# Kernel tuning notes

Measured on AMD Instinct MI355X. Metric: run time of the kernel, lower is better.

Reference implementation:

```python
import jax, jax.numpy as jnp
import numpy as np

N_NODES = 50000
N_EDGES = 640000
HID = 128


def _lin_params(key, out_dim, in_dim):
    kw, kb = jax.random.split(key)
    W = jax.random.normal(kw, (out_dim, in_dim), dtype=jnp.float32) * 0.02
    b = jax.random.normal(kb, (out_dim,), dtype=jnp.float32) * 0.02
    return W, b


def setup_inputs() -> dict:
    key = jax.random.key(0)
    ks = jax.random.split(key, 12)
    x = jax.random.normal(ks[0], (N_NODES, 3), dtype=jnp.float32)
    h = jax.random.normal(ks[1], (N_NODES, HID), dtype=jnp.float32)
    edge_index = jax.random.randint(ks[2], (2, N_EDGES), 0, N_NODES, dtype=jnp.int64)
    # edge_mlp: Linear(2H+1,H) -> SiLU -> Linear(H,H) -> SiLU -> Linear(H,H)
    ew1, eb1 = _lin_params(ks[3], HID, 2 * HID + 1)
    ew2, eb2 = _lin_params(ks[4], HID, HID)
    ew3, eb3 = _lin_params(ks[5], HID, HID)
    # coord_mlp: Linear(H,H) -> SiLU -> Linear(H,1)
    cw1, cb1 = _lin_params(ks[6], HID, HID)
    cw2, cb2 = _lin_params(ks[7], 1, HID)
    # node_mlp: Linear(2H,H) -> SiLU -> Linear(H,H) -> SiLU -> Linear(H,H)
    nw1, nb1 = _lin_params(ks[8], HID, 2 * HID)
    nw2, nb2 = _lin_params(ks[9], HID, HID)
    nw3, nb3 = _lin_params(ks[10], HID, HID)
    return {
        "x": x, "h": h, "edge_index": edge_index,
        "ew1": ew1, "eb1": eb1, "ew2": ew2, "eb2": eb2, "ew3": ew3, "eb3": eb3,
        "cw1": cw1, "cb1": cb1, "cw2": cw2, "cb2": cb2,
        "nw1": nw1, "nb1": nb1, "nw2": nw2, "nb2": nb2, "nw3": nw3, "nb3": nb3,
    }


def _lin(z, W, b):
    return z @ W.T + b


def _mlp3(z, W1, b1, W2, b2, W3, b3):
    z = jax.nn.silu(_lin(z, W1, b1))
    z = jax.nn.silu(_lin(z, W2, b2))
    return _lin(z, W3, b3)


def reference(x, h, edge_index,
              ew1, eb1, ew2, eb2, ew3, eb3,
              cw1, cb1, cw2, cb2,
              nw1, nb1, nw2, nb2, nw3, nb3):
    n = h.shape[0]
    src, dst = edge_index[0], edge_index[1]
    rel = x[src] - x[dst]                                   # [E, 3]
    d2 = jnp.sum(rel * rel, axis=-1, keepdims=True)         # [E, 1]
    e_in = jnp.concatenate([h[src], h[dst], d2], axis=-1)   # [E, 2H+1]
    m_ij = _mlp3(e_in, ew1, eb1, ew2, eb2, ew3, eb3)        # [E, H]
    m_aggr = jax.ops.segment_sum(m_ij, src, num_segments=n)  # [N, H]
    coord_coef = jnp.tanh(_lin(jax.nn.silu(_lin(m_ij, cw1, cb1)), cw2, cb2))  # [E, 1]
    delta_x = jax.ops.segment_sum(rel * coord_coef, src, num_segments=n)      # [N, 3]
    x_out = x + delta_x
    h_out = h + _mlp3(jnp.concatenate([h, m_aggr], axis=-1), nw1, nb1, nw2, nb2, nw3, nb3)
    return (x_out, h_out)
```

## Files before the change

### kernel.cpp

```cpp
#include <hip/hip_runtime.h>
#include <hip/hip_bf16.h>

#define N_NODES 50000
#define N_EDGES 640000
#define HID 128

typedef unsigned short ushort_t;
typedef __attribute__((ext_vector_type(8))) short bf16x8;
typedef __attribute__((ext_vector_type(4))) float f32x4;

#define U_MAGGR 0
#define U_HB    6400000
#define U_W1B   12800000
#define U_W2B   12832768
#define U_W3B   12849152
#define U_C1B   12865536
#define U_N1B   12881920
#define U_N2B   12914688
#define U_N3B   12931072
#define U_W1D2  12947456

__device__ __forceinline__ float silu_f(float v) {
    const float e = __builtin_amdgcn_exp2f(v * -1.442695041f);
    return v * __builtin_amdgcn_rcpf(1.0f + e);
}

__device__ __forceinline__ ushort_t f2b(float f) {
    __hip_bfloat16 b = __float2bfloat16(f);
    return __builtin_bit_cast(ushort_t, b);
}
__device__ __forceinline__ float b2f(ushort_t u) {
    union { float f; unsigned int i; } v; v.i = ((unsigned int)u) << 16; return v.f;
}
__device__ __forceinline__ float u2f(unsigned int u) {
    union { float f; unsigned int i; } v; v.i = u; return v.f;
}
__device__ __forceinline__ unsigned int pack2(float a, float b) {
    return (unsigned int)f2b(a) | ((unsigned int)f2b(b) << 16);
}
__device__ __forceinline__ void up8(const uint4& u, float* f) {
    f[0] = u2f(u.x << 16); f[1] = u2f(u.x & 0xffff0000u);
    f[2] = u2f(u.y << 16); f[3] = u2f(u.y & 0xffff0000u);
    f[4] = u2f(u.z << 16); f[5] = u2f(u.z & 0xffff0000u);
    f[6] = u2f(u.w << 16); f[7] = u2f(u.w & 0xffff0000u);
}
__device__ __forceinline__ void atom_add_f32(float* p, float v) { unsafeAtomicAdd(p, v); }

__device__ __forceinline__ void atom_pk_bf16(ushort_t* p, unsigned int v) {
#if __has_builtin(__builtin_amdgcn_global_atomic_fadd_v2bf16)
    typedef __attribute__((ext_vector_type(2))) short s2;
    s2 sv = __builtin_bit_cast(s2, v);
    __builtin_amdgcn_global_atomic_fadd_v2bf16((__attribute__((address_space(1))) s2*)p, sv);
#else
    unsigned int* up = (unsigned int*)p;
    unsigned int old = __hip_atomic_load(up, __ATOMIC_RELAXED, __HIP_MEMORY_SCOPE_AGENT), assumed;
    do {
        assumed = old;
        float lo = b2f((ushort_t)(assumed & 0xffff)) + b2f((ushort_t)(v & 0xffff));
        float hi = b2f((ushort_t)(assumed >> 16)) + b2f((ushort_t)(v >> 16));
        unsigned int nv = (unsigned int)f2b(lo) | ((unsigned int)f2b(hi) << 16);
        old = atomicCAS(up, assumed, nv);
    } while (old != assumed);
#endif
}

__global__ void prep_kernel(const float* __restrict__ x, const float* __restrict__ h,
                            const float* __restrict__ ew1, const float* __restrict__ ew2,
                            const float* __restrict__ ew3, const float* __restrict__ cw1,
                            const float* __restrict__ nw1, const float* __restrict__ nw2,
                            const float* __restrict__ nw3,
                            ushort_t* __restrict__ wsu, float* __restrict__ xout) {
    long i = (long)blockIdx.x * 256 + threadIdx.x;
    if (i < 3200000) { ((unsigned int*)(wsu + U_MAGGR))[i] = 0u; return; }
    i -= 3200000;
    if (i < 3200000) { ((unsigned int*)(wsu + U_HB))[i] = pack2(h[2 * i], h[2 * i + 1]); return; }
    i -= 3200000;
    if (i < 32768) {
        const int f = (int)(i >> 7);
        const int k = (int)(i & 127);
        const int src = (f < 128) ? (f * 257 + k) : ((f - 128) * 257 + 128 + k);
        wsu[U_W1B + i] = f2b(ew1[src]);
        return;
    }
    i -= 32768;
    if (i < 16384) { wsu[U_W2B + i] = f2b(ew2[i]); return; }
    i -= 16384;
    if (i < 16384) { wsu[U_W3B + i] = f2b(ew3[i]); return; }
    i -= 16384;
    if (i < 16384) { wsu[U_C1B + i] = f2b(cw1[i]); return; }
    i -= 16384;
    if (i < 32768) { wsu[U_N1B + i] = f2b(nw1[i]); return; }
    i -= 32768;
    if (i < 16384) { wsu[U_N2B + i] = f2b(nw2[i]); return; }
    i -= 16384;
    if (i < 16384) { wsu[U_N3B + i] = f2b(nw3[i]); return; }
    i -= 16384;
    if (i < 128) { ((float*)(wsu + U_W1D2))[i] = ew1[i * 257 + 256]; return; }
    i -= 128;
    if (i < 150000) xout[i] = x[i];
}

__global__ __launch_bounds__(256, 4) void ab_kernel(
    const ushort_t* __restrict__ hb, const ushort_t* __restrict__ wab,
    const float* __restrict__ eb1, ushort_t* __restrict__ abp) {
    __shared__ ushort_t sH[8192];
    const int t = threadIdx.x;
    const int lane = t & 63;
    const int wid = t >> 6;
    const int r15 = lane & 15;
    const int khi = lane >> 4;
    const int rhi = khi * 4;
    const int fb = wid * 64;
    const int n0 = blockIdx.x * 64;

    const uint4* hb4 = (const uint4*)hb;
#pragma unroll
    for (int it = 0; it < 4; ++it) {
        const int idx = it * 256 + t;
        const int e = idx >> 4, c = idx & 15;
        const int n = n0 + e;
        uint4 v = make_uint4(0u, 0u, 0u, 0u);
        if (n < N_NODES) v = hb4[(size_t)n * 16 + c];
        const int ui = (e * 128 + c * 8) ^ ((e & 7) << 3);
        *(uint4*)(sH + ui) = v;
    }
    __syncthreads();

    f32x4 acc[4][4];
#pragma unroll
    for (int mi = 0; mi < 4; ++mi)
#pragma unroll
        for (int ni = 0; ni < 4; ++ni) acc[mi][ni] = (f32x4){0.f, 0.f, 0.f, 0.f};
#pragma unroll
    for (int ks = 0; ks < 4; ++ks) {
        bf16x8 a[4];
#pragma unroll
        for (int mi = 0; mi < 4; ++mi)
            a[mi] = *(const bf16x8*)(wab + (fb + mi * 16 + r15) * 128 + ks * 32 + khi * 8);
        bf16x8 b[4];
#pragma unroll
        for (int ni = 0; ni < 4; ++ni) {
            const int e = ni * 16 + r15;
            const int ui = (e * 128 + ks * 32 + khi * 8) ^ ((e & 7) << 3);
            b[ni] = *(const bf16x8*)(sH + ui);
        }
#pragma unroll
        for (int mi = 0; mi < 4; ++mi)
#pragma unroll
            for (int ni = 0; ni < 4; ++ni)
                acc[mi][ni] = __builtin_amdgcn_mfma_f32_16x16x32_bf16(a[mi], b[ni], acc[mi][ni], 0, 0, 0);
    }

#pragma unroll
    for (int mi = 0; mi < 4; ++mi) {
        const int f0 = fb + mi * 16 + rhi;
        float4 bb = make_float4(0.f, 0.f, 0.f, 0.f);
        if (f0 >= 128) bb = *(const float4*)&eb1[f0 - 128];
#pragma unroll
        for (int ni = 0; ni < 4; ++ni) {
            const int n = n0 + ni * 16 + r15;
            if (n < N_NODES) {
                *(uint2*)(abp + (size_t)n * 256 + f0) =
                    make_uint2(pack2(acc[mi][ni][0] + bb.x, acc[mi][ni][1] + bb.y),
                               pack2(acc[mi][ni][2] + bb.z, acc[mi][ni][3] + bb.w));
            }
        }
    }
}

template <bool ACT>
__device__ __forceinline__ void dense128(ushort_t* sE, int srcBase, int dstBase,
                                         const ushort_t* __restrict__ W,
                                         const float* __restrict__ bias,
                                         int r15, int khi, int rhi, int fb) {
    f32x4 acc[4];
#pragma unroll
    for (int ni = 0; ni < 4; ++ni) acc[ni] = (f32x4){0.f, 0.f, 0.f, 0.f};
#pragma unroll
    for (int ks = 0; ks < 4; ++ks) {
        const bf16x8 a0 = *(const bf16x8*)(W + (fb + r15) * 128 + ks * 32 + khi * 8);
        bf16x8 b[4];
#pragma unroll
        for (int ni = 0; ni < 4; ++ni) {
            const int edge = ni * 16 + r15;
            const int ui = (srcBase + edge * 128 + ks * 32 + khi * 8) ^ ((edge & 7) << 3);
            b[ni] = *(const bf16x8*)(sE + ui);
        }
#pragma unroll
        for (int ni = 0; ni < 4; ++ni)
            acc[ni] = __builtin_amdgcn_mfma_f32_16x16x32_bf16(a0, b[ni], acc[ni], 0, 0, 0);
    }
    const float4 bb = *(const float4*)&bias[fb + rhi];
#pragma unroll
    for (int ni = 0; ni < 4; ++ni) {
        const int edge = ni * 16 + r15;
        float v0 = acc[ni][0] + bb.x;
        float v1 = acc[ni][1] + bb.y;
        float v2 = acc[ni][2] + bb.z;
        float v3 = acc[ni][3] + bb.w;
        if (ACT) { v0 = silu_f(v0); v1 = silu_f(v1); v2 = silu_f(v2); v3 = silu_f(v3); }
        const int ui = (dstBase + edge * 128 + fb + rhi) ^ ((edge & 7) << 3);
        *(uint2*)(sE + ui) = make_uint2(pack2(v0, v1), pack2(v2, v3));
    }
}

__global__ __launch_bounds__(512, 8) void edge_kernel(
    const float* __restrict__ x, const ushort_t* __restrict__ ab,
    const int* __restrict__ ei,
    const float* __restrict__ w1d2,
    const ushort_t* __restrict__ w2b, const float* __restrict__ eb2,
    const ushort_t* __restrict__ w3b, const float* __restrict__ eb3,
    const ushort_t* __restrict__ c1b, const float* __restrict__ cb1,
    const float* __restrict__ cw2, const float* __restrict__ cb2,
    float* __restrict__ xout, ushort_t* __restrict__ maggr) {
    __shared__ ushort_t sE[16384];
    __shared__ float srel[64][3];
    __shared__ float sd2[64];
    __shared__ int ssrc[64];
    __shared__ int sdst[64];

    const int t = threadIdx.x;
    const int lane = t & 63;
    const int wid = t >> 6;
    const int r15 = lane & 15;
    const int khi = lane >> 4;
    const int rhi = khi * 4;
    const int fb = wid * 16;
    const int e0 = blockIdx.x * 64;

    if (t < 64) {
        const int s = ei[e0 + t], d = ei[N_EDGES + e0 + t];
        ssrc[t] = s; sdst[t] = d;
        const float rx = x[3 * s] - x[3 * d];
        const float ry = x[3 * s + 1] - x[3 * d + 1];
        const float rz = x[3 * s + 2] - x[3 * d + 2];
        srel[t][0] = rx; srel[t][1] = ry; srel[t][2] = rz;
        sd2[t] = rx * rx + ry * ry + rz * rz;
    }
    __syncthreads();

    {
        const uint4* ab4 = (const uint4*)ab;
        uint4 va[2], vb[2];
        int ui[2], cc[2];
        float dd[2];
#pragma unroll
        for (int it = 0; it < 2; ++it) {
            const int idx = it * 512 + t;
            const int e = idx >> 4, c = idx & 15;
            va[it] = ab4[(size_t)ssrc[e] * 32 + c];
            vb[it] = ab4[(size_t)sdst[e] * 32 + 16 + c];
            dd[it] = sd2[e];
            cc[it] = c;
            ui[it] = (e * 128 + c * 8) ^ ((e & 7) << 3);
        }
#pragma unroll
        for (int it = 0; it < 2; ++it) {
            const int c8 = cc[it] * 8;
            const float4 w0 = *(const float4*)&w1d2[c8];
            const float4 w1 = *(const float4*)&w1d2[c8 + 4];
            const float d2 = dd[it];
            float fa[8], fbv[8];
            up8(va[it], fa);
            up8(vb[it], fbv);
            const float v0 = silu_f(fmaf(d2, w0.x, fa[0] + fbv[0]));
            const float v1 = silu_f(fmaf(d2, w0.y, fa[1] + fbv[1]));
            const float v2 = silu_f(fmaf(d2, w0.z, fa[2] + fbv[2]));
            const float v3 = silu_f(fmaf(d2, w0.w, fa[3] + fbv[3]));
            const float v4 = silu_f(fmaf(d2, w1.x, fa[4] + fbv[4]));
            const float v5 = silu_f(fmaf(d2, w1.y, fa[5] + fbv[5]));
            const float v6 = silu_f(fmaf(d2, w1.z, fa[6] + fbv[6]));
            const float v7 = silu_f(fmaf(d2, w1.w, fa[7] + fbv[7]));
            uint4 st;
            st.x = pack2(v0, v1); st.y = pack2(v2, v3);
            st.z = pack2(v4, v5); st.w = pack2(v6, v7);
            *(uint4*)(sE + ui[it]) = st;
        }
    }
    __syncthreads();

    dense128<true >(sE, 0, 8192, w2b, eb2, r15, khi, rhi, fb);
    __syncthreads();
    dense128<false>(sE, 8192, 0, w3b, eb3, r15, khi, rhi, fb);
    __syncthreads();
    dense128<true >(sE, 0, 8192, c1b, cb1, r15, khi, rhi, fb);
    __syncthreads();

    {
        const int esub = lane & 7;
        const int kg = lane >> 3;
        const int edge = wid * 8 + esub;
        float sum = 0.f;
#pragma unroll
        for (int cc = 0; cc < 2; ++cc) {
            const int k = kg * 16 + cc * 8;
            const int ui = (8192 + edge * 128 + k) ^ (esub << 3);
            const bf16x8 v = *(const bf16x8*)(sE + ui);
            const float4 ca = *(const float4*)&cw2[k];
            const float4 cb = *(const float4*)&cw2[k + 4];
            sum = fmaf(b2f((ushort_t)v[0]), ca.x, sum);
            sum = fmaf(b2f((ushort_t)v[1]), ca.y, sum);
            sum = fmaf(b2f((ushort_t)v[2]), ca.z, sum);
            sum = fmaf(b2f((ushort_t)v[3]), ca.w, sum);
            sum = fmaf(b2f((ushort_t)v[4]), cb.x, sum);
            sum = fmaf(b2f((ushort_t)v[5]), cb.y, sum);
            sum = fmaf(b2f((ushort_t)v[6]), cb.z, sum);
            sum = fmaf(b2f((ushort_t)v[7]), cb.w, sum);
        }
        sum += __shfl_xor(sum, 8);
        sum += __shfl_xor(sum, 16);
        sum += __shfl_xor(sum, 32);
        if (kg == 0) {
            const float coef = tanhf(sum + cb2[0]);
            const int s = ssrc[edge];
            atom_add_f32(&xout[3 * s + 0], srel[edge][0] * coef);
            atom_add_f32(&xout[3 * s + 1], srel[edge][1] * coef);
            atom_add_f32(&xout[3 * s + 2], srel[edge][2] * coef);
        }
    }

    {
        unsigned int v[8];
        size_t gaddr[8];
#pragma unroll
        for (int it = 0; it < 8; ++it) {
            const int idx = it * 512 + t;
            const int e = idx >> 6;
            const int dw = idx & 63;
            const int ui = (e * 128 + dw * 2) ^ ((e & 7) << 3);
            v[it] = *(const unsigned int*)(sE + ui);
            gaddr[it] = (size_t)ssrc[e] * 128 + dw * 2;
        }
#pragma unroll
        for (int it = 0; it < 8; ++it) atom_pk_bf16(maggr + gaddr[it], v[it]);
    }
}

__global__ __launch_bounds__(256, 4) void node_kernel(
    const float* __restrict__ h, const ushort_t* __restrict__ hb,
    const ushort_t* __restrict__ maggr,
    const ushort_t* __restrict__ n1b, const float* __restrict__ nb1,
    const ushort_t* __restrict__ n2b, const float* __restrict__ nb2,
    const ushort_t* __restrict__ n3b, const float* __restrict__ nb3,
    float* __restrict__ hout) {
    __shared__ ushort_t sE[16384];
    const int t = threadIdx.x;
    const int lane = t & 63;
    const int wid = t >> 6;
    const int r15 = lane & 15;
    const int khi = lane >> 4;
    const int rhi = khi * 4;
    const int fb = wid * 32;
    const int n0 = blockIdx.x * 64;

    const uint4* hb4 = (const uint4*)hb;
    const uint4* mg4 = (const uint4*)maggr;
#pragma unroll
    for (int it = 0; it < 8; ++it) {
        const int idx = it * 256 + t;
        const int e = idx >> 5, c = idx & 31;
        const int n = n0 + e;
        uint4 v = make_uint4(0u, 0u, 0u, 0u);
        if (n < N_NODES) v = (c < 16) ? hb4[(size_t)n * 16 + c] : mg4[(size_t)n * 16 + (c - 16)];
        const int ui = (e * 256 + c * 8) ^ ((e & 7) << 3);
        *(uint4*)(sE + ui) = v;
    }
    __syncthreads();

    f32x4 acc[2][4];
#pragma unroll
    for (int mi = 0; mi < 2; ++mi)
#pragma unroll
        for (int ni = 0; ni < 4; ++ni) acc[mi][ni] = (f32x4){0.f, 0.f, 0.f, 0.f};
#pragma unroll
    for (int ks = 0; ks < 8; ++ks) {
        const bf16x8 a0 = *(const bf16x8*)(n1b + (fb + r15) * 256 + ks * 32 + khi * 8);
        const bf16x8 a1 = *(const bf16x8*)(n1b + (fb + 16 + r15) * 256 + ks * 32 + khi * 8);
        bf16x8 b[4];
#pragma unroll
        for (int ni = 0; ni < 4; ++ni) {
            const int edge = ni * 16 + r15;
            const int ui = (edge * 256 + ks * 32 + khi * 8) ^ ((edge & 7) << 3);
            b[ni] = *(const bf16x8*)(sE + ui);
        }
#pragma unroll
        for (int ni = 0; ni < 4; ++ni) {
            acc[0][ni] = __builtin_amdgcn_mfma_f32_16x16x32_bf16(a0, b[ni], acc[0][ni], 0, 0, 0);
            acc[1][ni] = __builtin_amdgcn_mfma_f32_16x16x32_bf16(a1, b[ni], acc[1][ni], 0, 0, 0);
        }
    }
    __syncthreads();
    {
        const float4 bb0 = *(const float4*)&nb1[fb + rhi];
        const float4 bb1 = *(const float4*)&nb1[fb + 16 + rhi];
#pragma unroll
        for (int mi = 0; mi < 2; ++mi) {
            const float4 bb = mi ? bb1 : bb0;
#pragma unroll
            for (int ni = 0; ni < 4; ++ni) {
                const int edge = ni * 16 + r15;
                const float v0 = silu_f(acc[mi][ni][0] + bb.x);
                const float v1 = silu_f(acc[mi][ni][1] + bb.y);
                const float v2 = silu_f(acc[mi][ni][2] + bb.z);
                const float v3 = silu_f(acc[mi][ni][3] + bb.w);
                const int ui = (edge * 128 + fb + mi * 16 + rhi) ^ ((edge & 7) << 3);
                *(uint2*)(sE + ui) = make_uint2(pack2(v0, v1), pack2(v2, v3));
            }
        }
    }
    __syncthreads();

    {
#pragma unroll
        for (int half = 0; half < 2; ++half) {
            f32x4 a2[4];
#pragma unroll
            for (int ni = 0; ni < 4; ++ni) a2[ni] = (f32x4){0.f, 0.f, 0.f, 0.f};
            const int fbh = fb + half * 16;
#pragma unroll
            for (int ks = 0; ks < 4; ++ks) {
                const bf16x8 a0 = *(const bf16x8*)(n2b + (fbh + r15) * 128 + ks * 32 + khi * 8);
                bf16x8 b[4];
#pragma unroll
                for (int ni = 0; ni < 4; ++ni) {
                    const int edge = ni * 16 + r15;
                    const int ui = (edge * 128 + ks * 32 + khi * 8) ^ ((edge & 7) << 3);
                    b[ni] = *(const bf16x8*)(sE + ui);
                }
#pragma unroll
                for (int ni = 0; ni < 4; ++ni)
                    a2[ni] = __builtin_amdgcn_mfma_f32_16x16x32_bf16(a0, b[ni], a2[ni], 0, 0, 0);
            }
            const float4 bb = *(const float4*)&nb2[fbh + rhi];
#pragma unroll
            for (int ni = 0; ni < 4; ++ni) {
                const int edge = ni * 16 + r15;
                const float v0 = silu_f(a2[ni][0] + bb.x);
                const float v1 = silu_f(a2[ni][1] + bb.y);
                const float v2 = silu_f(a2[ni][2] + bb.z);
                const float v3 = silu_f(a2[ni][3] + bb.w);
                const int ui = (8192 + edge * 128 + fbh + rhi) ^ ((edge & 7) << 3);
                *(uint2*)(sE + ui) = make_uint2(pack2(v0, v1), pack2(v2, v3));
            }
        }
    }
    __syncthreads();

    {
        f32x4 a3[2][4];
#pragma unroll
        for (int mi = 0; mi < 2; ++mi)
#pragma unroll
            for (int ni = 0; ni < 4; ++ni) a3[mi][ni] = (f32x4){0.f, 0.f, 0.f, 0.f};
#pragma unroll
        for (int ks = 0; ks < 4; ++ks) {
            const bf16x8 a0 = *(const bf16x8*)(n3b + (fb + r15) * 128 + ks * 32 + khi * 8);
            const bf16x8 a1 = *(const bf16x8*)(n3b + (fb + 16 + r15) * 128 + ks * 32 + khi * 8);
            bf16x8 b[4];
#pragma unroll
            for (int ni = 0; ni < 4; ++ni) {
                const int edge = ni * 16 + r15;
                const int ui = (8192 + edge * 128 + ks * 32 + khi * 8) ^ ((edge & 7) << 3);
                b[ni] = *(const bf16x8*)(sE + ui);
            }
#pragma unroll
            for (int ni = 0; ni < 4; ++ni) {
                a3[0][ni] = __builtin_amdgcn_mfma_f32_16x16x32_bf16(a0, b[ni], a3[0][ni], 0, 0, 0);
                a3[1][ni] = __builtin_amdgcn_mfma_f32_16x16x32_bf16(a1, b[ni], a3[1][ni], 0, 0, 0);
            }
        }
        const float4 bb0 = *(const float4*)&nb3[fb + rhi];
        const float4 bb1 = *(const float4*)&nb3[fb + 16 + rhi];
#pragma unroll
        for (int mi = 0; mi < 2; ++mi) {
            const float4 bb = mi ? bb1 : bb0;
#pragma unroll
            for (int ni = 0; ni < 4; ++ni) {
                const int n = n0 + ni * 16 + r15;
                if (n < N_NODES) {
                    const size_t o = (size_t)n * 128 + fb + mi * 16 + rhi;
                    const float4 hv = *(const float4*)&h[o];
                    float4 ov;
                    ov.x = hv.x + a3[mi][ni][0] + bb.x;
                    ov.y = hv.y + a3[mi][ni][1] + bb.y;
                    ov.z = hv.z + a3[mi][ni][2] + bb.z;
                    ov.w = hv.w + a3[mi][ni][3] + bb.w;
                    *(float4*)&hout[o] = ov;
                }
            }
        }
    }
}

extern "C" void kernel_launch(void* const* d_in, const int* in_sizes, int n_in,
                              void* d_out, int out_size, void* d_ws, size_t ws_size,
                              hipStream_t stream) {
    const float* x   = (const float*)d_in[0];
    const float* h   = (const float*)d_in[1];
    const int*   ei  = (const int*)d_in[2];
    const float* ew1 = (const float*)d_in[3];
    const float* eb1 = (const float*)d_in[4];
    const float* ew2 = (const float*)d_in[5];
    const float* eb2 = (const float*)d_in[6];
    const float* ew3 = (const float*)d_in[7];
    const float* eb3 = (const float*)d_in[8];
    const float* cw1 = (const float*)d_in[9];
    const float* cb1 = (const float*)d_in[10];
    const float* cw2 = (const float*)d_in[11];
    const float* cb2 = (const float*)d_in[12];
    const float* nw1 = (const float*)d_in[13];
    const float* nb1 = (const float*)d_in[14];
    const float* nw2 = (const float*)d_in[15];
    const float* nb2 = (const float*)d_in[16];
    const float* nw3 = (const float*)d_in[17];
    const float* nb3 = (const float*)d_in[18];

    float* out  = (float*)d_out;
    float* xout = out;
    float* hout = out + (size_t)N_NODES * 3;
    ushort_t* wsu = (ushort_t*)d_ws;

    ushort_t* maggr = wsu + U_MAGGR;
    const ushort_t* hb  = wsu + U_HB;
    const ushort_t* wab = wsu + U_W1B;
    const ushort_t* w2b = wsu + U_W2B;
    const ushort_t* w3b = wsu + U_W3B;
    const ushort_t* c1b = wsu + U_C1B;
    const ushort_t* n1b = wsu + U_N1B;
    const ushort_t* n2b = wsu + U_N2B;
    const ushort_t* n3b = wsu + U_N3B;
    const float* w1d2 = (const float*)(wsu + U_W1D2);

    ushort_t* abp = (ushort_t*)hout;

    const long prep_total = 3200000L + 3200000L + 32768 + 3 * 16384 + 32768 + 2 * 16384 + 128 + 150000;
    const int prep_blocks = (int)((prep_total + 255) / 256);
    prep_kernel<<<prep_blocks, 256, 0, stream>>>(x, h, ew1, ew2, ew3, cw1, nw1, nw2, nw3,
                                                 wsu, xout);

    ab_kernel<<<(N_NODES + 63) / 64, 256, 0, stream>>>(hb, wab, eb1, abp);

    edge_kernel<<<N_EDGES / 64, 512, 0, stream>>>(x, abp, ei,
                                                  w1d2, w2b, eb2, w3b, eb3,
                                                  c1b, cb1, cw2, cb2,
                                                  xout, maggr);

    node_kernel<<<(N_NODES + 63) / 64, 256, 0, stream>>>(h, hb, maggr,
                                                         n1b, nb1, n2b, nb2, n3b, nb3,
                                                         hout);
}
```

Before: 315.6 us.

## Fold edge layer-3 weights into coord MLP and scatter messages straight from MFMA accumulators

Since m_ij = W3·z + b3 feeds the coord MLP linearly, the change precomputes Wc = C1·W3 and bc = C1·b3 + cb1 in an extra block of ab_kernel. That lets the edge kernel compute the W3 layer and the coord layer from the same layer-2 activations without a dependent round trip through shared memory. The layer-3 output is atomically added to maggr directly from the MFMA accumulators, and the coord dot product is reduced in registers with a small shared partial buffer instead of a separate LDS pass. Edge index and gather loads are also issued before the first barrier to overlap latency. The cost is an extra block with a 128x128 matmul, a larger LDS footprint in ab_kernel, and slightly different bf16 rounding for the coord path.

```diff
diff --git a/kernel.cpp b/kernel.cpp
--- a/kernel.cpp
+++ b/kernel.cpp
@@ -19,6 +19,8 @@
 #define U_N2B   12914688
 #define U_N3B   12931072
 #define U_W1D2  12947456
+#define U_WC    12947712
+#define U_BC    12964096
 
 __device__ __forceinline__ float silu_f(float v) {
     const float e = __builtin_amdgcn_exp2f(v * -1.442695041f);
@@ -102,14 +104,68 @@
 
 __global__ __launch_bounds__(256, 4) void ab_kernel(
     const ushort_t* __restrict__ hb, const ushort_t* __restrict__ wab,
-    const float* __restrict__ eb1, ushort_t* __restrict__ abp) {
-    __shared__ ushort_t sH[8192];
+    const float* __restrict__ eb1, ushort_t* __restrict__ abp,
+    const ushort_t* __restrict__ c1b, const float* __restrict__ ew3,
+    const float* __restrict__ eb3, const float* __restrict__ cb1,
+    ushort_t* __restrict__ wcb, float* __restrict__ bcv, int nAB) {
+    __shared__ ushort_t sH[16384];
     const int t = threadIdx.x;
     const int lane = t & 63;
     const int wid = t >> 6;
     const int r15 = lane & 15;
     const int khi = lane >> 4;
     const int rhi = khi * 4;
+
+    if ((int)blockIdx.x == nAB) {
+        for (int i = t; i < 16384; i += 256) {
+            const int m = i >> 7, k = i & 127;
+            sH[(k * 128 + m) ^ ((k & 7) << 3)] = f2b(ew3[i]);
+        }
+        __syncthreads();
+#pragma unroll
+        for (int kh = 0; kh < 2; ++kh) {
+#pragma unroll
+            for (int fi = 0; fi < 2; ++fi) {
+                const int f0 = wid * 32 + fi * 16;
+                const int kc = kh * 64;
+                f32x4 acc[4];
+#pragma unroll
+                for (int ni = 0; ni < 4; ++ni) acc[ni] = (f32x4){0.f, 0.f, 0.f, 0.f};
+#pragma unroll
+                for (int ks = 0; ks < 4; ++ks) {
+                    const bf16x8 a0 = *(const bf16x8*)(c1b + (f0 + r15) * 128 + ks * 32 + khi * 8);
+                    bf16x8 b[4];
+#pragma unroll
+                    for (int ni = 0; ni < 4; ++ni) {
+                        const int kk = kc + ni * 16 + r15;
+                        b[ni] = *(const bf16x8*)(sH + ((kk * 128 + ks * 32 + khi * 8) ^ ((kk & 7) << 3)));
+                    }
+#pragma unroll
+                    for (int ni = 0; ni < 4; ++ni)
+                        acc[ni] = __builtin_amdgcn_mfma_f32_16x16x32_bf16(a0, b[ni], acc[ni], 0, 0, 0);
+                }
+#pragma unroll
+                for (int ni = 0; ni < 4; ++ni) {
+                    const int kk = kc + ni * 16 + r15;
+#pragma unroll
+                    for (int j = 0; j < 4; ++j)
+                        wcb[(f0 + rhi + j) * 128 + kk] = f2b(acc[ni][j]);
+                }
+            }
+        }
+        {
+            const int f = t >> 1, hf = t & 1;
+            float s = 0.f;
+            const int m0 = hf * 64;
+#pragma unroll 8
+            for (int m = m0; m < m0 + 64; ++m)
+                s = fmaf(b2f(c1b[f * 128 + m]), eb3[m], s);
+            s += __shfl_xor(s, 1);
+            if (hf == 0) bcv[f] = cb1[f] + s;
+        }
+        return;
+    }
+
     const int fb = wid * 64;
     const int n0 = blockIdx.x * 64;
 
@@ -210,14 +266,14 @@
     const float* __restrict__ w1d2,
     const ushort_t* __restrict__ w2b, const float* __restrict__ eb2,
     const ushort_t* __restrict__ w3b, const float* __restrict__ eb3,
-    const ushort_t* __restrict__ c1b, const float* __restrict__ cb1,
+    const ushort_t* __restrict__ wcb, const float* __restrict__ bcv,
     const float* __restrict__ cw2, const float* __restrict__ cb2,
     float* __restrict__ xout, ushort_t* __restrict__ maggr) {
     __shared__ ushort_t sE[16384];
     __shared__ float srel[64][3];
     __shared__ float sd2[64];
     __shared__ int ssrc[64];
-    __shared__ int sdst[64];
+    __shared__ float sPart[8][64];
 
     const int t = threadIdx.x;
     const int lane = t & 63;
@@ -228,9 +284,25 @@
     const int fb = wid * 16;
     const int e0 = blockIdx.x * 64;
 
+    uint4 va[2], vb[2];
+    int ui[2], ee[2];
+    {
+        const uint4* ab4 = (const uint4*)ab;
+#pragma unroll
+        for (int it = 0; it < 2; ++it) {
+            const int idx = it * 512 + t;
+            const int e = idx >> 4, c = idx & 15;
+            const int s = ei[e0 + e];
+            const int d = ei[N_EDGES + e0 + e];
+            va[it] = ab4[(size_t)s * 32 + c];
+            vb[it] = ab4[(size_t)d * 32 + 16 + c];
+            ee[it] = e;
+            ui[it] = (e * 128 + c * 8) ^ ((e & 7) << 3);
+        }
+    }
     if (t < 64) {
         const int s = ei[e0 + t], d = ei[N_EDGES + e0 + t];
-        ssrc[t] = s; sdst[t] = d;
+        ssrc[t] = s;
         const float rx = x[3 * s] - x[3 * d];
         const float ry = x[3 * s + 1] - x[3 * d + 1];
         const float rz = x[3 * s + 2] - x[3 * d + 2];
@@ -239,100 +311,113 @@
     }
     __syncthreads();
 
+#pragma unroll
+    for (int it = 0; it < 2; ++it) {
+        const int c8 = ((it * 512 + t) & 15) * 8;
+        const float4 w0 = *(const float4*)&w1d2[c8];
+        const float4 w1 = *(const float4*)&w1d2[c8 + 4];
+        const float d2 = sd2[ee[it]];
+        float fa[8], fbv[8];
+        up8(va[it], fa);
+        up8(vb[it], fbv);
+        const float v0 = silu_f(fmaf(d2, w0.x, fa[0] + fbv[0]));
+        const float v1 = silu_f(fmaf(d2, w0.y, fa[1] + fbv[1]));
+        const float v2 = silu_f(fmaf(d2, w0.z, fa[2] + fbv[2]));
+        const float v3 = silu_f(fmaf(d2, w0.w, fa[3] + fbv[3]));
+        const float v4 = silu_f(fmaf(d2, w1.x, fa[4] + fbv[4]));
+        const float v5 = silu_f(fmaf(d2, w1.y, fa[5] + fbv[5]));
+        const float v6 = silu_f(fmaf(d2, w1.z, fa[6] + fbv[6]));
+        const float v7 = silu_f(fmaf(d2, w1.w, fa[7] + fbv[7]));
+        uint4 st;
+        st.x = pack2(v0, v1); st.y = pack2(v2, v3);
+        st.z = pack2(v4, v5); st.w = pack2(v6, v7);
+        *(uint4*)(sE + ui[it]) = st;
+    }
+    __syncthreads();
+
+    dense128<true>(sE, 0, 8192, w2b, eb2, r15, khi, rhi, fb);
+    __syncthreads();
+
     {
-        const uint4* ab4 = (const uint4*)ab;
-        uint4 va[2], vb[2];
-        int ui[2], cc[2];
-        float dd[2];
-#pragma unroll
-        for (int it = 0; it < 2; ++it) {
-            const int idx = it * 512 + t;
-            const int e = idx >> 4, c = idx & 15;
-            va[it] = ab4[(size_t)ssrc[e] * 32 + c];
-            vb[it] = ab4[(size_t)sdst[e] * 32 + 16 + c];
-            dd[it] = sd2[e];
-            cc[it] = c;
-            ui[it] = (e * 128 + c * 8) ^ ((e & 7) << 3);
-        }
-#pragma unroll
-        for (int it = 0; it < 2; ++it) {
-            const int c8 = cc[it] * 8;
-            const float4 w0 = *(const float4*)&w1d2[c8];
-            const float4 w1 = *(const float4*)&w1d2[c8 + 4];
-            const float d2 = dd[it];
-            float fa[8], fbv[8];
-            up8(va[it], fa);
-            up8(vb[it], fbv);
-            const float v0 = silu_f(fmaf(d2, w0.x, fa[0] + fbv[0]));
-            const float v1 = silu_f(fmaf(d2, w0.y, fa[1] + fbv[1]));
-            const float v2 = silu_f(fmaf(d2, w0.z, fa[2] + fbv[2]));
-            const float v3 = silu_f(fmaf(d2, w0.w, fa[3] + fbv[3]));
-            const float v4 = silu_f(fmaf(d2, w1.x, fa[4] + fbv[4]));
-            const float v5 = silu_f(fmaf(d2, w1.y, fa[5] + fbv[5]));
-            const float v6 = silu_f(fmaf(d2, w1.z, fa[6] + fbv[6]));
-            const float v7 = silu_f(fmaf(d2, w1.w, fa[7] + fbv[7]));
-            uint4 st;
-            st.x = pack2(v0, v1); st.y = pack2(v2, v3);
-            st.z = pack2(v4, v5); st.w = pack2(v6, v7);
-            *(uint4*)(sE + ui[it]) = st;
-        }
-    }
-    __syncthreads();
-
-    dense128<true >(sE, 0, 8192, w2b, eb2, r15, khi, rhi, fb);
-    __syncthreads();
-    dense128<false>(sE, 8192, 0, w3b, eb3, r15, khi, rhi, fb);
-    __syncthreads();
-    dense128<true >(sE, 0, 8192, c1b, cb1, r15, khi, rhi, fb);
-    __syncthreads();
+        f32x4 acc[4];
+#pragma unroll
+        for (int ni = 0; ni < 4; ++ni) acc[ni] = (f32x4){0.f, 0.f, 0.f, 0.f};
+#pragma unroll
+        for (int ks = 0; ks < 4; ++ks) {
+            const bf16x8 a0 = *(const bf16x8*)(w3b + (fb + r15) * 128 + ks * 32 + khi * 8);
+            bf16x8 b[4];
+#pragma unroll
+            for (int ni = 0; ni < 4; ++ni) {
+                const int edge = ni * 16 + r15;
+                const int u = (8192 + edge * 128 + ks * 32 + khi * 8) ^ ((edge & 7) << 3);
+                b[ni] = *(const bf16x8*)(sE + u);
+            }
+#pragma unroll
+            for (int ni = 0; ni < 4; ++ni)
+                acc[ni] = __builtin_amdgcn_mfma_f32_16x16x32_bf16(a0, b[ni], acc[ni], 0, 0, 0);
+        }
+        const float4 bb = *(const float4*)&eb3[fb + rhi];
+#pragma unroll
+        for (int ni = 0; ni < 4; ++ni) {
+            const int edge = ni * 16 + r15;
+            const unsigned int w0 = pack2(acc[ni][0] + bb.x, acc[ni][1] + bb.y);
+            const unsigned int w1 = pack2(acc[ni][2] + bb.z, acc[ni][3] + bb.w);
+            const size_t g = (size_t)ssrc[edge] * 128 + fb + rhi;
+            atom_pk_bf16(maggr + g, w0);
+            atom_pk_bf16(maggr + g + 2, w1);
+        }
+    }
 
     {
-        const int esub = lane & 7;
-        const int kg = lane >> 3;
-        const int edge = wid * 8 + esub;
-        float sum = 0.f;
-#pragma unroll
-        for (int cc = 0; cc < 2; ++cc) {
-            const int k = kg * 16 + cc * 8;
-            const int ui = (8192 + edge * 128 + k) ^ (esub << 3);
-            const bf16x8 v = *(const bf16x8*)(sE + ui);
-            const float4 ca = *(const float4*)&cw2[k];
-            const float4 cb = *(const float4*)&cw2[k + 4];
-            sum = fmaf(b2f((ushort_t)v[0]), ca.x, sum);
-            sum = fmaf(b2f((ushort_t)v[1]), ca.y, sum);
-            sum = fmaf(b2f((ushort_t)v[2]), ca.z, sum);
-            sum = fmaf(b2f((ushort_t)v[3]), ca.w, sum);
-            sum = fmaf(b2f((ushort_t)v[4]), cb.x, sum);
-            sum = fmaf(b2f((ushort_t)v[5]), cb.y, sum);
-            sum = fmaf(b2f((ushort_t)v[6]), cb.z, sum);
-            sum = fmaf(b2f((ushort_t)v[7]), cb.w, sum);
-        }
-        sum += __shfl_xor(sum, 8);
-        sum += __shfl_xor(sum, 16);
-        sum += __shfl_xor(sum, 32);
-        if (kg == 0) {
-            const float coef = tanhf(sum + cb2[0]);
-            const int s = ssrc[edge];
-            atom_add_f32(&xout[3 * s + 0], srel[edge][0] * coef);
-            atom_add_f32(&xout[3 * s + 1], srel[edge][1] * coef);
-            atom_add_f32(&xout[3 * s + 2], srel[edge][2] * coef);
-        }
-    }
-
-    {
-        unsigned int v[8];
-        size_t gaddr[8];
-#pragma unroll
-        for (int it = 0; it < 8; ++it) {
-            const int idx = it * 512 + t;
-            const int e = idx >> 6;
-            const int dw = idx & 63;
-            const int ui = (e * 128 + dw * 2) ^ ((e & 7) << 3);
-            v[it] = *(const unsigned int*)(sE + ui);
-            gaddr[it] = (size_t)ssrc[e] * 128 + dw * 2;
-        }
-#pragma unroll
-        for (int it = 0; it < 8; ++it) atom_pk_bf16(maggr + gaddr[it], v[it]);
+        f32x4 acc[4];
+#pragma unroll
+        for (int ni = 0; ni < 4; ++ni) acc[ni] = (f32x4){0.f, 0.f, 0.f, 0.f};
+#pragma unroll
+        for (int ks = 0; ks < 4; ++ks) {
+            const bf16x8 a0 = *(const bf16x8*)(wcb + (fb + r15) * 128 + ks * 32 + khi * 8);
+            bf16x8 b[4];
+#pragma unroll
+            for (int ni = 0; ni < 4; ++ni) {
+                const int edge = ni * 16 + r15;
+                const int u = (8192 + edge * 128 + ks * 32 + khi * 8) ^ ((edge & 7) << 3);
+                b[ni] = *(const bf16x8*)(sE + u);
+            }
+#pragma unroll
+            for (int ni = 0; ni < 4; ++ni)
+                acc[ni] = __builtin_amdgcn_mfma_f32_16x16x32_bf16(a0, b[ni], acc[ni], 0, 0, 0);
+        }
+        const float4 bb = *(const float4*)&bcv[fb + rhi];
+        const float4 cw = *(const float4*)&cw2[fb + rhi];
+        float p[4];
+#pragma unroll
+        for (int ni = 0; ni < 4; ++ni) {
+            float s = silu_f(acc[ni][0] + bb.x) * cw.x;
+            s = fmaf(silu_f(acc[ni][1] + bb.y), cw.y, s);
+            s = fmaf(silu_f(acc[ni][2] + bb.z), cw.z, s);
+            s = fmaf(silu_f(acc[ni][3] + bb.w), cw.w, s);
+            p[ni] = s;
+        }
+#pragma unroll
+        for (int ni = 0; ni < 4; ++ni) {
+            p[ni] += __shfl_xor(p[ni], 16);
+            p[ni] += __shfl_xor(p[ni], 32);
+        }
+        if (khi == 0) {
+#pragma unroll
+            for (int ni = 0; ni < 4; ++ni) sPart[wid][ni * 16 + r15] = p[ni];
+        }
+    }
+    __syncthreads();
+
+    if (t < 64) {
+        float s = sPart[0][t];
+#pragma unroll
+        for (int w = 1; w < 8; ++w) s += sPart[w][t];
+        const float coef = tanhf(s + cb2[0]);
+        const int sn = ssrc[t];
+        atom_add_f32(&xout[3 * sn + 0], srel[t][0] * coef);
+        atom_add_f32(&xout[3 * sn + 1], srel[t][1] * coef);
+        atom_add_f32(&xout[3 * sn + 2], srel[t][2] * coef);
     }
 }
 
@@ -530,6 +615,8 @@
     const ushort_t* n2b = wsu + U_N2B;
     const ushort_t* n3b = wsu + U_N3B;
     const float* w1d2 = (const float*)(wsu + U_W1D2);
+    ushort_t* wcb = wsu + U_WC;
+    float* bcv = (float*)(wsu + U_BC);
 
     ushort_t* abp = (ushort_t*)hout;
 
@@ -538,11 +625,13 @@
     prep_kernel<<<prep_blocks, 256, 0, stream>>>(x, h, ew1, ew2, ew3, cw1, nw1, nw2, nw3,
                                                  wsu, xout);
 
-    ab_kernel<<<(N_NODES + 63) / 64, 256, 0, stream>>>(hb, wab, eb1, abp);
+    const int nAB = (N_NODES + 63) / 64;
+    ab_kernel<<<nAB + 1, 256, 0, stream>>>(hb, wab, eb1, abp,
+                                           c1b, ew3, eb3, cb1, wcb, bcv, nAB);
 
     edge_kernel<<<N_EDGES / 64, 512, 0, stream>>>(x, abp, ei,
                                                   w1d2, w2b, eb2, w3b, eb3,
-                                                  c1b, cb1, cw2, cb2,
+                                                  wcb, bcv, cw2, cb2,
                                                   xout, maggr);
 
     node_kernel<<<(N_NODES + 63) / 64, 256, 0, stream>>>(h, hb, maggr,
```

After: 722.1 us. 2.29x slower.
